# Optimization experiments

Measured on AMD Instinct MI355X. Metric: run time of the kernel, lower is better.

The kernel has to match this reference:

```python
import jax, jax.numpy as jnp
import numpy as np

SE_TEMP = 0.2
BN_EPS = 1e-5

def _l2n(x):
    # F.normalize(p=2, dim=-1) with eps=1e-12 clamp on the norm
    n = jnp.linalg.norm(x, axis=-1, keepdims=True)
    return x / jnp.maximum(n, 1e-12)

def setup_inputs() -> dict:
    key = jax.random.key(0)
    k1, k2, k3, k4, k5 = jax.random.split(key, 5)
    Q, I, D = 256, 2048, 256
    return {
        "query_feats": jax.random.normal(k1, (Q, D), dtype=jnp.float32),
        "query_img_feats": jax.random.normal(k2, (Q, D), dtype=jnp.float32),
        "gallery_img_feats": jax.random.normal(k3, (I, D), dtype=jnp.float32),
        "bn_gamma": jnp.ones((D,), dtype=jnp.float32),
        "bn_beta": jnp.zeros((D,), dtype=jnp.float32),
        "bn_mean": jax.random.normal(k4, (D,), dtype=jnp.float32) * 0.1,
        "bn_var": jax.random.uniform(k5, (D,), dtype=jnp.float32, minval=0.5, maxval=1.5),
    }

def reference(query_feats, query_img_feats, gallery_img_feats, bn_gamma, bn_beta, bn_mean, bn_var):
    # GalleryFilterNetwork.get_scores, mode='combined', gfn_activation_mode='se'
    inv_std = bn_gamma / jnp.sqrt(bn_var + BN_EPS)

    def bn(x):  # eval-mode BatchNorm1d over last dim D
        return (x - bn_mean) * inv_std + bn_beta

    xq = _l2n(query_feats)        # [Q, D] normalized query box feats
    yq = _l2n(query_img_feats)    # [Q, D] normalized query scene feats
    yg = _l2n(gallery_img_feats)  # [I, D] normalized gallery scene feats

    gate = jax.nn.sigmoid(xq / SE_TEMP)           # [Q, D]
    fused_query = bn(yq * gate)                   # [Q, D]  (non-p SE fuse)
    fused_gal = bn(yg[:, None, :] * gate[None])   # [I, Q, D] (p=True SE fuse)

    # cosine similarity per (q, i) pair, then sigmoid
    scores = jax.nn.sigmoid(
        jnp.einsum('qd,iqd->qi', _l2n(fused_query), _l2n(fused_gal))
    )
    return scores  # [Q, I]
```

## Files before the change

kernel.cpp:

```cpp
#include <hip/hip_runtime.h>
#include <math.h>

#define D 256
#define Q 256
#define I 2048

typedef __attribute__((ext_vector_type(8))) short short8;
typedef __attribute__((ext_vector_type(4))) float floatx4;

__device__ __forceinline__ float wave_sum(float v) {
#pragma unroll
    for (int off = 1; off < 64; off <<= 1)
        v += __shfl_xor(v, off, 64);
    return v;
}

__device__ __forceinline__ float sigmoidf_(float x) {
    return 1.0f / (1.0f + expf(-x));
}

__device__ __forceinline__ unsigned short f2bf(float f) {
    unsigned u = __float_as_uint(f);
    u += 0x7FFFu + ((u >> 16) & 1u);
    return (unsigned short)(u >> 16);
}

__global__ void __launch_bounds__(256)
prep(const float* __restrict__ qf,
     const float* __restrict__ qif,
     const float* __restrict__ gal,
     const float* __restrict__ gamma,
     const float* __restrict__ beta,
     const float* __restrict__ mean,
     const float* __restrict__ var,
     unsigned short* __restrict__ PB,
     unsigned short* __restrict__ WB,
     unsigned short* __restrict__ VB,
     unsigned short* __restrict__ YB,
     unsigned short* __restrict__ Y2B,
     float* __restrict__ sq,
     float* __restrict__ ccp) {
    const int t = threadIdx.x;
    const int wv = t >> 6, l = t & 63;

    if (blockIdx.x >= 64) {
        const int i = (blockIdx.x - 64) * 4 + wv;
        float4 x = ((const float4*)gal)[(size_t)i * 64 + l];
        float n = wave_sum(x.x * x.x + x.y * x.y + x.z * x.z + x.w * x.w);
        float inv = 1.0f / fmaxf(sqrtf(n), 1e-12f);
        float y0 = x.x * inv, y1 = x.y * inv, y2 = x.z * inv, y3 = x.w * inv;
        *(ushort4*)&YB[(size_t)i * D + 4 * l] =
            make_ushort4(f2bf(y0), f2bf(y1), f2bf(y2), f2bf(y3));
        *(ushort4*)&Y2B[(size_t)i * D + 4 * l] =
            make_ushort4(f2bf(y0 * y0), f2bf(y1 * y1), f2bf(y2 * y2), f2bf(y3 * y3));
        return;
    }

    const int q = blockIdx.x * 4 + wv;
    const float4* qf4  = (const float4*)qf;
    const float4* qif4 = (const float4*)qif;
    const float4* ga4  = (const float4*)gamma;
    const float4* be4  = (const float4*)beta;
    const float4* me4  = (const float4*)mean;
    const float4* va4  = (const float4*)var;

    float4 x = qf4[(size_t)q * 64 + l];
    float nx = wave_sum(x.x * x.x + x.y * x.y + x.z * x.z + x.w * x.w);
    float inx = 1.0f / fmaxf(sqrtf(nx), 1e-12f);
    float g0 = sigmoidf_(x.x * inx * 5.0f);
    float g1 = sigmoidf_(x.y * inx * 5.0f);
    float g2 = sigmoidf_(x.z * inx * 5.0f);
    float g3 = sigmoidf_(x.w * inx * 5.0f);

    float4 y = qif4[(size_t)q * 64 + l];
    float ny = wave_sum(y.x * y.x + y.y * y.y + y.z * y.z + y.w * y.w);
    float iny = 1.0f / fmaxf(sqrtf(ny), 1e-12f);

    float4 gm = ga4[l], bt = be4[l], mn = me4[l], vr = va4[l];
    float is0 = gm.x * rsqrtf(vr.x + 1e-5f);
    float is1 = gm.y * rsqrtf(vr.y + 1e-5f);
    float is2 = gm.z * rsqrtf(vr.z + 1e-5f);
    float is3 = gm.w * rsqrtf(vr.w + 1e-5f);
    float c0 = bt.x - mn.x * is0;
    float c1 = bt.y - mn.y * is1;
    float c2 = bt.z - mn.z * is2;
    float c3 = bt.w - mn.w * is3;
    float a0 = g0 * is0, a1 = g1 * is1, a2 = g2 * is2, a3 = g3 * is3;

    float f0 = y.x * iny * a0 + c0;
    float f1 = y.y * iny * a1 + c1;
    float f2 = y.z * iny * a2 + c2;
    float f3 = y.w * iny * a3 + c3;
    float nf = wave_sum(f0 * f0 + f1 * f1 + f2 * f2 + f3 * f3);
    float inf_ = 1.0f / fmaxf(sqrtf(nf), 1e-12f);
    float u0 = f0 * inf_, u1 = f1 * inf_, u2 = f2 * inf_, u3 = f3 * inf_;

    *(ushort4*)&PB[(size_t)q * D + 4 * l] =
        make_ushort4(f2bf(u0 * a0), f2bf(u1 * a1), f2bf(u2 * a2), f2bf(u3 * a3));
    *(ushort4*)&WB[(size_t)q * D + 4 * l] =
        make_ushort4(f2bf(a0 * a0), f2bf(a1 * a1), f2bf(a2 * a2), f2bf(a3 * a3));
    *(ushort4*)&VB[(size_t)q * D + 4 * l] =
        make_ushort4(f2bf(2.0f * a0 * c0), f2bf(2.0f * a1 * c1),
                     f2bf(2.0f * a2 * c2), f2bf(2.0f * a3 * c3));

    float s = wave_sum(u0 * c0 + u1 * c1 + u2 * c2 + u3 * c3);
    if (l == 0) sq[q] = s;

    if (q == 0) {
        float ccs = wave_sum(c0 * c0 + c1 * c1 + c2 * c2 + c3 * c3);
        if (l == 0) *ccp = ccs;
    }
}

__global__ void __launch_bounds__(64)
main_scores(const unsigned short* __restrict__ YB,
            const unsigned short* __restrict__ Y2B,
            const unsigned short* __restrict__ PB,
            const unsigned short* __restrict__ WB,
            const unsigned short* __restrict__ VB,
            const float* __restrict__ sq,
            const float* __restrict__ ccp,
            float* __restrict__ out) {
    const int l = threadIdx.x;
    const int lm = l & 15, quad = l >> 4, koff = quad * 8;
    const int q0 = blockIdx.x * 16, i0 = blockIdx.y * 32;
    const int qr = q0 + lm;

    short8 bp[8], bw[8], bv[8];
#pragma unroll
    for (int ks = 0; ks < 8; ks++) {
        const size_t o = (size_t)qr * D + ks * 32 + koff;
        bp[ks] = *(const short8*)&PB[o];
        bw[ks] = *(const short8*)&WB[o];
        bv[ks] = *(const short8*)&VB[o];
    }
    const float sqv = sq[qr];
    const float ccv = *ccp;

#pragma unroll
    for (int it = 0; it < 2; it++) {
        const int ir = i0 + it * 16 + lm;
        floatx4 acc1 = {0.f, 0.f, 0.f, 0.f};
        floatx4 acc2 = {0.f, 0.f, 0.f, 0.f};
#pragma unroll
        for (int ks = 0; ks < 8; ks++) {
            const size_t o = (size_t)ir * D + ks * 32 + koff;
            short8 ay  = *(const short8*)&YB[o];
            short8 ay2 = *(const short8*)&Y2B[o];
            acc1 = __builtin_amdgcn_mfma_f32_16x16x32_bf16(ay,  bp[ks], acc1, 0, 0, 0);
            acc2 = __builtin_amdgcn_mfma_f32_16x16x32_bf16(ay2, bw[ks], acc2, 0, 0, 0);
            acc2 = __builtin_amdgcn_mfma_f32_16x16x32_bf16(ay,  bv[ks], acc2, 0, 0, 0);
        }
        float4 o4;
        float* po = &o4.x;
#pragma unroll
        for (int rr = 0; rr < 4; rr++) {
            float nrm = fmaxf(sqrtf(fmaxf(acc2[rr] + ccv, 0.f)), 1e-12f);
            po[rr] = sigmoidf_((acc1[rr] + sqv) / nrm);
        }
        *(float4*)&out[(size_t)qr * I + i0 + it * 16 + quad * 4] = o4;
    }
}

extern "C" void kernel_launch(void* const* d_in, const int* in_sizes, int n_in,
                              void* d_out, int out_size, void* d_ws, size_t ws_size,
                              hipStream_t stream) {
    const float* qf    = (const float*)d_in[0];
    const float* qif   = (const float*)d_in[1];
    const float* gal   = (const float*)d_in[2];
    const float* gamma = (const float*)d_in[3];
    const float* beta  = (const float*)d_in[4];
    const float* mean  = (const float*)d_in[5];
    const float* var   = (const float*)d_in[6];
    float* out = (float*)d_out;

    char* base = (char*)d_ws;
    float* sq = (float*)base;
    float* cc = (float*)(base + 1024);
    unsigned short* PB = (unsigned short*)(base + 2048);
    unsigned short* WB = PB + (size_t)Q * D;
    unsigned short* VB = WB + (size_t)Q * D;
    unsigned short* YB = VB + (size_t)Q * D;
    unsigned short* Y2B = YB + (size_t)I * D;

    prep<<<576, 256, 0, stream>>>(qf, qif, gal, gamma, beta, mean, var,
                                  PB, WB, VB, YB, Y2B, sq, cc);
    main_scores<<<dim3(Q / 16, I / 32), 64, 0, stream>>>(YB, Y2B, PB, WB, VB,
                                                         sq, cc, out);
}
```

Baseline: 78.09 us.

## Fuse prep and scoring kernels into one cooperative launch with grid sync

Merges the preprocessing kernel and the MFMA scoring kernel into a single cooperative kernel of 1024 single-wave blocks. Each block normalizes two gallery rows and, for the first 256 blocks, one query row, then calls a grid-wide sync before computing its 16x32 score tile. This removes one kernel launch and the gap between the two dependent launches. In exchange it adds grid-barrier cost, needs all 1024 blocks to be co-resident, and runs the prep phase with 64-thread blocks.

```diff
diff --git a/kernel.cpp b/kernel.cpp
--- a/kernel.cpp
+++ b/kernel.cpp
@@ -1,9 +1,12 @@
 #include <hip/hip_runtime.h>
+#include <hip/hip_cooperative_groups.h>
 #include <math.h>
 
 #define D 256
 #define Q 256
 #define I 2048
+
+namespace cg = cooperative_groups;
 
 typedef __attribute__((ext_vector_type(8))) short short8;
 typedef __attribute__((ext_vector_type(4))) float floatx4;
@@ -25,26 +28,28 @@
     return (unsigned short)(u >> 16);
 }
 
-__global__ void __launch_bounds__(256)
-prep(const float* __restrict__ qf,
-     const float* __restrict__ qif,
-     const float* __restrict__ gal,
-     const float* __restrict__ gamma,
-     const float* __restrict__ beta,
-     const float* __restrict__ mean,
-     const float* __restrict__ var,
-     unsigned short* __restrict__ PB,
-     unsigned short* __restrict__ WB,
-     unsigned short* __restrict__ VB,
-     unsigned short* __restrict__ YB,
-     unsigned short* __restrict__ Y2B,
-     float* __restrict__ sq,
-     float* __restrict__ ccp) {
-    const int t = threadIdx.x;
-    const int wv = t >> 6, l = t & 63;
+__global__ void __launch_bounds__(64)
+gfn_fused(const float* __restrict__ qf,
+          const float* __restrict__ qif,
+          const float* __restrict__ gal,
+          const float* __restrict__ gamma,
+          const float* __restrict__ beta,
+          const float* __restrict__ mean,
+          const float* __restrict__ var,
+          unsigned short* __restrict__ PB,
+          unsigned short* __restrict__ WB,
+          unsigned short* __restrict__ VB,
+          unsigned short* __restrict__ YB,
+          unsigned short* __restrict__ Y2B,
+          float* __restrict__ sq,
+          float* __restrict__ ccp,
+          float* __restrict__ out) {
+    const int b = blockIdx.x;
+    const int l = threadIdx.x;
 
-    if (blockIdx.x >= 64) {
-        const int i = (blockIdx.x - 64) * 4 + wv;
+#pragma unroll
+    for (int r = 0; r < 2; r++) {
+        const int i = b * 2 + r;
         float4 x = ((const float4*)gal)[(size_t)i * 64 + l];
         float n = wave_sum(x.x * x.x + x.y * x.y + x.z * x.z + x.w * x.w);
         float inv = 1.0f / fmaxf(sqrtf(n), 1e-12f);
@@ -53,77 +58,69 @@
             make_ushort4(f2bf(y0), f2bf(y1), f2bf(y2), f2bf(y3));
         *(ushort4*)&Y2B[(size_t)i * D + 4 * l] =
             make_ushort4(f2bf(y0 * y0), f2bf(y1 * y1), f2bf(y2 * y2), f2bf(y3 * y3));
-        return;
     }
 
-    const int q = blockIdx.x * 4 + wv;
-    const float4* qf4  = (const float4*)qf;
-    const float4* qif4 = (const float4*)qif;
-    const float4* ga4  = (const float4*)gamma;
-    const float4* be4  = (const float4*)beta;
-    const float4* me4  = (const float4*)mean;
-    const float4* va4  = (const float4*)var;
+    if (b < Q) {
+        const int q = b;
+        const float4* qf4  = (const float4*)qf;
+        const float4* qif4 = (const float4*)qif;
+        const float4* ga4  = (const float4*)gamma;
+        const float4* be4  = (const float4*)beta;
+        const float4* me4  = (const float4*)mean;
+        const float4* va4  = (const float4*)var;
 
-    float4 x = qf4[(size_t)q * 64 + l];
-    float nx = wave_sum(x.x * x.x + x.y * x.y + x.z * x.z + x.w * x.w);
-    float inx = 1.0f / fmaxf(sqrtf(nx), 1e-12f);
-    float g0 = sigmoidf_(x.x * inx * 5.0f);
-    float g1 = sigmoidf_(x.y * inx * 5.0f);
-    float g2 = sigmoidf_(x.z * inx * 5.0f);
-    float g3 = sigmoidf_(x.w * inx * 5.0f);
+        float4 x = qf4[(size_t)q * 64 + l];
+        float nx = wave_sum(x.x * x.x + x.y * x.y + x.z * x.z + x.w * x.w);
+        float inx = 1.0f / fmaxf(sqrtf(nx), 1e-12f);
+        float g0 = sigmoidf_(x.x * inx * 5.0f);
+        float g1 = sigmoidf_(x.y * inx * 5.0f);
+        float g2 = sigmoidf_(x.z * inx * 5.0f);
+        float g3 = sigmoidf_(x.w * inx * 5.0f);
 
-    float4 y = qif4[(size_t)q * 64 + l];
-    float ny = wave_sum(y.x * y.x + y.y * y.y + y.z * y.z + y.w * y.w);
-    float iny = 1.0f / fmaxf(sqrtf(ny), 1e-12f);
+        float4 y = qif4[(size_t)q * 64 + l];
+        float ny = wave_sum(y.x * y.x + y.y * y.y + y.z * y.z + y.w * y.w);
+        float iny = 1.0f / fmaxf(sqrtf(ny), 1e-12f);
 
-    float4 gm = ga4[l], bt = be4[l], mn = me4[l], vr = va4[l];
-    float is0 = gm.x * rsqrtf(vr.x + 1e-5f);
-    float is1 = gm.y * rsqrtf(vr.y + 1e-5f);
-    float is2 = gm.z * rsqrtf(vr.z + 1e-5f);
-    float is3 = gm.w * rsqrtf(vr.w + 1e-5f);
-    float c0 = bt.x - mn.x * is0;
-    float c1 = bt.y - mn.y * is1;
-    float c2 = bt.z - mn.z * is2;
-    float c3 = bt.w - mn.w * is3;
-    float a0 = g0 * is0, a1 = g1 * is1, a2 = g2 * is2, a3 = g3 * is3;
+        float4 gm = ga4[l], bt = be4[l], mn = me4[l], vr = va4[l];
+        float is0 = gm.x * rsqrtf(vr.x + 1e-5f);
+        float is1 = gm.y * rsqrtf(vr.y + 1e-5f);
+        float is2 = gm.z * rsqrtf(vr.z + 1e-5f);
+        float is3 = gm.w * rsqrtf(vr.w + 1e-5f);
+        float c0 = bt.x - mn.x * is0;
+        float c1 = bt.y - mn.y * is1;
+        float c2 = bt.z - mn.z * is2;
+        float c3 = bt.w - mn.w * is3;
+        float a0 = g0 * is0, a1 = g1 * is1, a2 = g2 * is2, a3 = g3 * is3;
 
-    float f0 = y.x * iny * a0 + c0;
-    float f1 = y.y * iny * a1 + c1;
-    float f2 = y.z * iny * a2 + c2;
-    float f3 = y.w * iny * a3 + c3;
-    float nf = wave_sum(f0 * f0 + f1 * f1 + f2 * f2 + f3 * f3);
-    float inf_ = 1.0f / fmaxf(sqrtf(nf), 1e-12f);
-    float u0 = f0 * inf_, u1 = f1 * inf_, u2 = f2 * inf_, u3 = f3 * inf_;
+        float f0 = y.x * iny * a0 + c0;
+        float f1 = y.y * iny * a1 + c1;
+        float f2 = y.z * iny * a2 + c2;
+        float f3 = y.w * iny * a3 + c3;
+        float nf = wave_sum(f0 * f0 + f1 * f1 + f2 * f2 + f3 * f3);
+        float inf_ = 1.0f / fmaxf(sqrtf(nf), 1e-12f);
+        float u0 = f0 * inf_, u1 = f1 * inf_, u2 = f2 * inf_, u3 = f3 * inf_;
 
-    *(ushort4*)&PB[(size_t)q * D + 4 * l] =
-        make_ushort4(f2bf(u0 * a0), f2bf(u1 * a1), f2bf(u2 * a2), f2bf(u3 * a3));
-    *(ushort4*)&WB[(size_t)q * D + 4 * l] =
-        make_ushort4(f2bf(a0 * a0), f2bf(a1 * a1), f2bf(a2 * a2), f2bf(a3 * a3));
-    *(ushort4*)&VB[(size_t)q * D + 4 * l] =
-        make_ushort4(f2bf(2.0f * a0 * c0), f2bf(2.0f * a1 * c1),
-                     f2bf(2.0f * a2 * c2), f2bf(2.0f * a3 * c3));
+        *(ushort4*)&PB[(size_t)q * D + 4 * l] =
+            make_ushort4(f2bf(u0 * a0), f2bf(u1 * a1), f2bf(u2 * a2), f2bf(u3 * a3));
+        *(ushort4*)&WB[(size_t)q * D + 4 * l] =
+            make_ushort4(f2bf(a0 * a0), f2bf(a1 * a1), f2bf(a2 * a2), f2bf(a3 * a3));
+        *(ushort4*)&VB[(size_t)q * D + 4 * l] =
+            make_ushort4(f2bf(2.0f * a0 * c0), f2bf(2.0f * a1 * c1),
+                         f2bf(2.0f * a2 * c2), f2bf(2.0f * a3 * c3));
 
-    float s = wave_sum(u0 * c0 + u1 * c1 + u2 * c2 + u3 * c3);
-    if (l == 0) sq[q] = s;
+        float s = wave_sum(u0 * c0 + u1 * c1 + u2 * c2 + u3 * c3);
+        if (l == 0) sq[q] = s;
 
-    if (q == 0) {
-        float ccs = wave_sum(c0 * c0 + c1 * c1 + c2 * c2 + c3 * c3);
-        if (l == 0) *ccp = ccs;
+        if (q == 0) {
+            float ccs = wave_sum(c0 * c0 + c1 * c1 + c2 * c2 + c3 * c3);
+            if (l == 0) *ccp = ccs;
+        }
     }
-}
 
-__global__ void __launch_bounds__(64)
-main_scores(const unsigned short* __restrict__ YB,
-            const unsigned short* __restrict__ Y2B,
-            const unsigned short* __restrict__ PB,
-            const unsigned short* __restrict__ WB,
-            const unsigned short* __restrict__ VB,
-            const float* __restrict__ sq,
-            const float* __restrict__ ccp,
-            float* __restrict__ out) {
-    const int l = threadIdx.x;
+    cg::this_grid().sync();
+
     const int lm = l & 15, quad = l >> 4, koff = quad * 8;
-    const int q0 = blockIdx.x * 16, i0 = blockIdx.y * 32;
+    const int q0 = (b & 15) * 16, i0 = (b >> 4) * 32;
     const int qr = q0 + lm;
 
     short8 bp[8], bw[8], bv[8];
@@ -183,8 +180,8 @@
     unsigned short* YB = VB + (size_t)Q * D;
     unsigned short* Y2B = YB + (size_t)I * D;
 
-    prep<<<576, 256, 0, stream>>>(qf, qif, gal, gamma, beta, mean, var,
-                                  PB, WB, VB, YB, Y2B, sq, cc);
-    main_scores<<<dim3(Q / 16, I / 32), 64, 0, stream>>>(YB, Y2B, PB, WB, VB,
-                                                         sq, cc, out);
+    void* args[] = {&qf, &qif, &gal, &gamma, &beta, &mean, &var,
+                    &PB, &WB, &VB, &YB, &Y2B, &sq, &cc, &out};
+    hipLaunchCooperativeKernel((void*)gfn_fused, dim3(1024), dim3(64),
+                               args, 0, stream);
 }
```

Result: slower. 168.3 us (+115.5%).
